# Performance work log

Measured on AMD Instinct MI355X. Metric: run time of the kernel, lower is better.

## Reference

```python
import jax, jax.numpy as jnp
import numpy as np

V = 50000
E = 800000
B, FIN, FOUT, K = 2, 64, 64, 4


def setup_inputs() -> dict:
    key = jax.random.key(0)
    k1, k2, k3, k4, k5, k6 = jax.random.split(key, 6)
    inputs = jax.random.normal(k1, (B, V, FIN), dtype=jnp.float32)
    weight = jax.random.normal(k2, (K, FIN, FOUT), dtype=jnp.float32) * np.sqrt(2.0 / (FIN * K)).astype(np.float32)
    bias = jax.random.normal(k3, (FOUT,), dtype=jnp.float32)
    lap_vals = jax.random.normal(k4, (E,), dtype=jnp.float32)
    lap_rows = jax.random.randint(k5, (E,), 0, V, dtype=jnp.int32)
    lap_cols = jax.random.randint(k6, (E,), 0, V, dtype=jnp.int32)
    return {"inputs": inputs, "weight": weight, "bias": bias,
            "lap_vals": lap_vals, "lap_rows": lap_rows, "lap_cols": lap_cols}


def reference(inputs, weight, bias, lap_vals, lap_rows, lap_cols):
    B_, V_, Fin = inputs.shape
    K_, _, Fout = weight.shape

    def spmm(x):  # L @ x, L in COO; x: [V, Fin*B]
        return jax.ops.segment_sum(lap_vals[:, None] * x[lap_cols], lap_rows, num_segments=V_)

    # x0: [V, Fin*B] (Fin-major flatten, matching torch permute(1,2,0).view)
    x0 = jnp.transpose(inputs, (1, 2, 0)).reshape(V_, Fin * B_)
    xs = [x0]
    if K_ > 1:
        x1 = spmm(x0)
        xs.append(x1)
        for _ in range(2, K_):
            x2 = 2.0 * spmm(x1) - x0
            xs.append(x2)
            x0, x1 = x1, x2
    # [K,V,Fin,B] -> [B,V,Fin,K] -> [B*V, Fin*K]
    X = jnp.stack(xs).reshape(K_, V_, Fin, B_)
    X = jnp.transpose(X, (3, 1, 2, 0)).reshape(B_ * V_, Fin * K_)
    # faithful to original: weight flattened as (K*Fin, Fout)
    out = X @ weight.reshape(K_ * Fin, Fout)
    return out.reshape(B_, V_, Fout) + bias
```

## Files before the change

kernel.cpp:

```cpp
#include <hip/hip_runtime.h>
#include <hip/hip_bf16.h>


#define NV 50000
#define NE 800000
#define XROW 128
#define NROWS 100000
#define NTILES 6250
#define EPMAX 1700000
#define BSHIFT 7
#define RPB 128
#define NB 391
#define CAP 3072
#define CHUNK 4096
#define P1_BLOCKS 196
#define X0_BLOCKS 12500

using u16 = unsigned short;
using u32 = unsigned int;
using u64 = unsigned long long;
typedef __bf16 bf16x8 __attribute__((ext_vector_type(8)));
typedef float f32x4 __attribute__((ext_vector_type(4)));

__device__ __forceinline__ float bflo(u32 g) { return __uint_as_float(g << 16); }
__device__ __forceinline__ float bfhi(u32 g) { return __uint_as_float(g & 0xffff0000u); }
__device__ __forceinline__ u32 pack_bf2(float a, float b) {
    u16 ha = __builtin_bit_cast(u16, (__bf16)a);
    u16 hb = __builtin_bit_cast(u16, (__bf16)b);
    return (u32)ha | ((u32)hb << 16);
}
__device__ __forceinline__ float unpack_f16hi(u32 rec) {
    u16 h = (u16)(rec >> 16);
    return (float)__builtin_bit_cast(_Float16, h);
}
__device__ __forceinline__ int pad32(int n) { return (n + 31) & ~31; }

__global__ __launch_bounds__(256) void bin1_k(const int* __restrict__ rows, const int* __restrict__ cols,
                                              const float* __restrict__ vals,
                                              int* __restrict__ binctr, u64* __restrict__ tmp) {
    __shared__ int bcnt[NB];
    __shared__ int bofs[NB];
    __shared__ int bcur[NB];
    __shared__ int gbase[NB];
    __shared__ int ps[256];
    __shared__ u64 stage[CHUNK];
    int t = threadIdx.x;
    int base = blockIdx.x * CHUNK;
    int n = NE - base;
    if (n > CHUNK) n = CHUNK;
    if (n <= 0) return;

    for (int i = t; i < NB; i += 256) bcnt[i] = 0;
    __syncthreads();

    for (int i = t; i < n; i += 256) {
        atomicAdd(&bcnt[rows[base + i] >> BSHIFT], 1);
    }
    __syncthreads();

    int i0 = 2 * t, i1 = 2 * t + 1;
    int a0 = (i0 < NB) ? bcnt[i0] : 0;
    int a1 = (i1 < NB) ? bcnt[i1] : 0;
    ps[t] = a0 + a1;
    __syncthreads();
    for (int off = 1; off < 256; off <<= 1) {
        int v = (t >= off) ? ps[t - off] : 0;
        __syncthreads();
        ps[t] += v;
        __syncthreads();
    }
    int eb = ps[t] - (a0 + a1);
    if (i0 < NB) { bofs[i0] = eb;      bcur[i0] = eb;      gbase[i0] = i0 * CAP + atomicAdd(&binctr[i0], a0); }
    if (i1 < NB) { bofs[i1] = eb + a0; bcur[i1] = eb + a0; gbase[i1] = i1 * CAP + atomicAdd(&binctr[i1], a1); }
    __syncthreads();

    for (int i = t; i < n; i += 256) {
        int r = rows[base + i];
        int c = cols[base + i];
        u16 hv = __builtin_bit_cast(u16, (_Float16)vals[base + i]);
        u64 rec = ((u64)(u32)r << 32) | (u64)((u32)c | ((u32)hv << 16));
        int s = atomicAdd(&bcur[r >> BSHIFT], 1);
        stage[s] = rec;
    }
    __syncthreads();

    for (int i = t; i < n; i += 256) {
        u64 rec = stage[i];
        int b = (int)(rec >> (32 + BSHIFT));
        tmp[(size_t)(gbase[b] + (i - bofs[b]))] = rec;
    }
}

__global__ __launch_bounds__(256) void bcnt_k(const u64* __restrict__ tmp, const int* __restrict__ binctr,
                                              int* __restrict__ rowc, int* __restrict__ btot,
                                              int* __restrict__ done,
                                              int* __restrict__ bbase, int* __restrict__ row_ptr) {
    __shared__ int rc[RPB];
    __shared__ int rs[RPB];
    __shared__ int ps[256];
    __shared__ int flag;
    int b = blockIdx.x, t = threadIdx.x;
    int n = binctr[b];
    const u64* rec = tmp + (size_t)b * CAP;
    if (t < RPB) rc[t] = 0;
    __syncthreads();
    for (int i = t; i < n; i += 256) {
        atomicAdd(&rc[(int)(rec[i] >> 32) & (RPB - 1)], 1);
    }
    __syncthreads();
    if (t < RPB) {
        rowc[b * RPB + t] = rc[t];
        rs[t] = pad32(rc[t]);
    }
    __syncthreads();
    for (int off = 64; off > 0; off >>= 1) {
        if (t < off) rs[t] += rs[t + off];
        __syncthreads();
    }
    if (t == 0) {
        btot[b] = rs[0];
        __threadfence();
        int ticket = atomicAdd(done, 1);
        flag = (ticket == NB - 1);
    }
    __syncthreads();
    if (flag) {
        __threadfence();
        int i0 = 2 * t, i1 = 2 * t + 1;
        int a0 = (i0 < NB) ? atomicAdd(&btot[i0], 0) : 0;
        int a1 = (i1 < NB) ? atomicAdd(&btot[i1], 0) : 0;
        ps[t] = a0 + a1;
        __syncthreads();
        for (int off = 1; off < 256; off <<= 1) {
            int v = (t >= off) ? ps[t - off] : 0;
            __syncthreads();
            ps[t] += v;
            __syncthreads();
        }
        int eb = ps[t] - (a0 + a1);
        if (i0 < NB) bbase[i0] = eb;
        if (i1 < NB) bbase[i1] = eb + a0;
        if (t == 255) row_ptr[NV] = ps[255];
    }
}

__global__ __launch_bounds__(256) void place_k(const u64* __restrict__ tmp, const int* __restrict__ binctr,
                                               const int* __restrict__ rowc, const int* __restrict__ bbase,
                                               int* __restrict__ row_ptr, u32* __restrict__ epack) {
    __shared__ int rc[RPB];
    __shared__ int ro[RPB];
    int b = blockIdx.x, t = threadIdx.x;
    int n = binctr[b];
    int base = bbase[b];
    const u64* rec = tmp + (size_t)b * CAP;

    int cv = (t < RPB) ? rowc[b * RPB + t] : 0;
    int pv = pad32(cv);
    if (t < RPB) ro[t] = pv;
    __syncthreads();
    for (int off = 1; off < RPB; off <<= 1) {
        int v = 0;
        if (t < RPB && t >= off) v = ro[t - off];
        __syncthreads();
        if (t < RPB) ro[t] += v;
        __syncthreads();
    }
    if (t < RPB) {
        int ex = ro[t] - pv;
        ro[t] = ex;
        rc[t] = 0;
        int v = (b << BSHIFT) + t;
        if (v < NV) row_ptr[v] = base + ex;
    }
    __syncthreads();
    for (int i = t; i < n; i += 256) {
        u64 r64 = rec[i];
        int r = (int)(r64 >> 32) & (RPB - 1);
        int p = base + ro[r] + atomicAdd(&rc[r], 1);
        epack[p] = (u32)r64;
    }
    __syncthreads();
    if (t < RPB) {
        int s = base + ro[t] + cv;
        int e = base + ro[t] + pv;
        for (int i = s; i < e; ++i) epack[i] = 0;
    }
}

__global__ void bx0w_k(const float* __restrict__ in, u32* __restrict__ x0u,
                       const float* __restrict__ weight, u16* __restrict__ wimg) {
    int bid = blockIdx.x;
    if (bid < X0_BLOCKS) {
        int i = bid * 256 + threadIdx.x;
        int v = i >> 6, p = i & 63;
        int b = p >> 5;
        int f = (p & 31) * 2;
        const float* src = in + (size_t)b * (NV * 64) + (size_t)v * 64 + f;
        float2 t = *(const float2*)src;
        x0u[i] = pack_bf2(t.x, t.y);
    } else {
        int i = (bid - X0_BLOCKS) * 256 + threadIdx.x;
        int c = i >> 6, o = i & 63;
        int cp = ((c & 3) << 6) | (c >> 2);
        wimg[o * 264 + cp] = __builtin_bit_cast(u16, (__bf16)weight[i]);
    }
}

__global__ __launch_bounds__(256) void spmm_k(const u32* __restrict__ x,
                                              const u32* __restrict__ xprev,
                                              const int* __restrict__ row_ptr,
                                              const u32* __restrict__ epack,
                                              u32* __restrict__ xout, int mode) {
    int wave = (int)((blockIdx.x * blockDim.x + threadIdx.x) >> 6);
    u32 lane = threadIdx.x & 63;
    int row = __builtin_amdgcn_readfirstlane(wave);
    if (row >= NV) return;
    int beg = row_ptr[row];
    int end = row_ptr[row + 1];
    int q = (int)(lane >> 4);
    u32 g16 = lane & 15;

    float ax[4] = {0.f, 0.f, 0.f, 0.f};
    float ay[4] = {0.f, 0.f, 0.f, 0.f};

    for (int e = beg; e < end; e += 32) {
        u32 rec[8];
        #pragma unroll
        for (int u = 0; u < 8; ++u) rec[u] = epack[e + 4 * u + q];
        uint4 gv[8];
        #pragma unroll
        for (int u = 0; u < 8; ++u)
            gv[u] = *(const uint4*)(x + ((rec[u] & 0xffffu) << 6) + (g16 << 2));
        #pragma unroll
        for (int u = 0; u < 8; ++u) {
            float w = unpack_f16hi(rec[u]);
            ax[0] += w * bflo(gv[u].x); ay[0] += w * bfhi(gv[u].x);
            ax[1] += w * bflo(gv[u].y); ay[1] += w * bfhi(gv[u].y);
            ax[2] += w * bflo(gv[u].z); ay[2] += w * bfhi(gv[u].z);
            ax[3] += w * bflo(gv[u].w); ay[3] += w * bfhi(gv[u].w);
        }
    }

    #pragma unroll
    for (int m = 16; m <= 32; m <<= 1) {
        #pragma unroll
        for (int j = 0; j < 4; ++j) {
            ax[j] += __shfl_xor(ax[j], m, 64);
            ay[j] += __shfl_xor(ay[j], m, 64);
        }
    }

    if (q == 0) {
        if (mode) {
            uint4 pv = *(const uint4*)(xprev + ((u32)row << 6) + (g16 << 2));
            ax[0] = 2.f * ax[0] - bflo(pv.x); ay[0] = 2.f * ay[0] - bfhi(pv.x);
            ax[1] = 2.f * ax[1] - bflo(pv.y); ay[1] = 2.f * ay[1] - bfhi(pv.y);
            ax[2] = 2.f * ax[2] - bflo(pv.z); ay[2] = 2.f * ay[2] - bfhi(pv.z);
            ax[3] = 2.f * ax[3] - bflo(pv.w); ay[3] = 2.f * ay[3] - bfhi(pv.w);
        }
        uint4 o;
        o.x = pack_bf2(ax[0], ay[0]);
        o.y = pack_bf2(ax[1], ay[1]);
        o.z = pack_bf2(ax[2], ay[2]);
        o.w = pack_bf2(ax[3], ay[3]);
        *(uint4*)(xout + ((u32)row << 6) + (g16 << 2)) = o;
    }
}

__global__ __launch_bounds__(256) void final_k(const u16* __restrict__ x_all,
                                               const u16* __restrict__ wimg,
                                               const float* __restrict__ bias,
                                               float* __restrict__ out) {
    __shared__ u16 Wt[64 * 264];
    {
        const u32* src = (const u32*)wimg;
        u32* dst = (u32*)Wt;
        #pragma unroll 4
        for (int i = threadIdx.x; i < 64 * 264 / 2; i += 256) dst[i] = src[i];
    }
    __syncthreads();

    int lane = threadIdx.x & 63;
    int wid = threadIdx.x >> 6;
    int pair = blockIdx.x * 4 + wid;
    int t0 = pair * 2;
    if (t0 >= NTILES) return;

    int m = lane & 15;
    int q8 = (lane >> 4) * 8;

    int r0 = t0 * 16 + m;
    int r1 = r0 + 16;
    const u16* arow0 = x_all + (size_t)(r0 >> 1) * XROW + (r0 & 1) * 64;
    const u16* arow1 = x_all + (size_t)(r1 >> 1) * XROW + (r1 & 1) * 64;

    f32x4 accA[4] = {{0,0,0,0},{0,0,0,0},{0,0,0,0},{0,0,0,0}};
    f32x4 accB[4] = {{0,0,0,0},{0,0,0,0},{0,0,0,0},{0,0,0,0}};

    #pragma unroll
    for (int kb = 0; kb < 8; ++kb) {
        int cb = kb * 32 + q8;
        int arr = cb >> 6;
        int f0 = cb & 63;
        size_t aoff = (size_t)arr * (NV * XROW) + f0;
        bf16x8 a0 = *(const bf16x8*)(arow0 + aoff);
        bf16x8 a1 = *(const bf16x8*)(arow1 + aoff);
        #pragma unroll
        for (int j = 0; j < 4; ++j) {
            bf16x8 bj = *(const bf16x8*)&Wt[(j * 16 + m) * 264 + kb * 32 + q8];
            accA[j] = __builtin_amdgcn_mfma_f32_16x16x32_bf16(a0, bj, accA[j], 0, 0, 0);
            accB[j] = __builtin_amdgcn_mfma_f32_16x16x32_bf16(a1, bj, accB[j], 0, 0, 0);
        }
    }

    float bv[4];
    #pragma unroll
    for (int j = 0; j < 4; ++j) bv[j] = bias[j * 16 + m];

    #pragma unroll
    for (int half = 0; half < 2; ++half) {
        int rbase = (t0 + half) * 16 + (lane >> 4) * 4;
        f32x4* acc = half ? accB : accA;
        #pragma unroll
        for (int reg = 0; reg < 4; ++reg) {
            int rr = rbase + reg;
            float* op = out + (size_t)(rr & 1) * (NV * 64) + (size_t)(rr >> 1) * 64;
            #pragma unroll
            for (int j = 0; j < 4; ++j) op[j * 16 + m] = acc[j][reg] + bv[j];
        }
    }
}

extern "C" void kernel_launch(void* const* d_in, const int* in_sizes, int n_in,
                              void* d_out, int out_size, void* d_ws, size_t ws_size,
                              hipStream_t stream) {
    const float* inputs = (const float*)d_in[0];
    const float* weight = (const float*)d_in[1];
    const float* bias   = (const float*)d_in[2];
    const float* lapv   = (const float*)d_in[3];
    const int*   lrows  = (const int*)d_in[4];
    const int*   lcols  = (const int*)d_in[5];
    float* out = (float*)d_out;

    char* ws = (char*)d_ws;
    size_t o = 0;
    auto alloc = [&](size_t bytes) -> void* {
        void* p = ws + o;
        o += (bytes + 255) & ~(size_t)255;
        return p;
    };
    u16* x_all = (u16*)alloc((size_t)4 * NV * XROW * 2);
    u32* epack = (u32*)alloc((size_t)EPMAX * 4);
    u64* tmp   = (u64*)alloc((size_t)NB * CAP * 8);
    int* row_ptr = (int*)alloc((size_t)(NV + 1) * 4);
    int* binctr  = (int*)alloc((size_t)(NB + 1) * 4);
    int* btot    = (int*)alloc((size_t)NB * 4);
    int* bbase   = (int*)alloc((size_t)NB * 4);
    int* rowc    = (int*)alloc((size_t)NB * RPB * 4);
    u16* wimg = (u16*)alloc((size_t)64 * 264 * 2);
    (void)ws_size; (void)in_sizes; (void)n_in; (void)out_size;

    int* done = binctr + NB;

    u32* x0 = (u32*)(x_all + (size_t)0 * NV * XROW);
    u32* x1 = (u32*)(x_all + (size_t)1 * NV * XROW);
    u32* x2 = (u32*)(x_all + (size_t)2 * NV * XROW);
    u32* x3 = (u32*)(x_all + (size_t)3 * NV * XROW);

    hipMemsetAsync(binctr, 0, (size_t)(NB + 1) * 4, stream);
    bin1_k<<<P1_BLOCKS, 256, 0, stream>>>(lrows, lcols, lapv, binctr, tmp);
    bcnt_k<<<NB, 256, 0, stream>>>(tmp, binctr, rowc, btot, done, bbase, row_ptr);
    place_k<<<NB, 256, 0, stream>>>(tmp, binctr, rowc, bbase, row_ptr, epack);
    bx0w_k<<<X0_BLOCKS + 64, 256, 0, stream>>>(inputs, x0, weight, wimg);

    spmm_k<<<(NV + 3) / 4, 256, 0, stream>>>(x0, nullptr, row_ptr, epack, x1, 0);
    spmm_k<<<(NV + 3) / 4, 256, 0, stream>>>(x1, x0, row_ptr, epack, x2, 1);
    spmm_k<<<(NV + 3) / 4, 256, 0, stream>>>(x2, x1, row_ptr, epack, x3, 1);

    final_k<<<(NTILES / 2 + 3) / 4, 256, 0, stream>>>(x_all, wimg, bias, out);
}
```

Before: 234.8 us.

## Fuse three SpMM passes into one cooperative kernel with grid sync

```diff
diff --git a/kernel.cpp b/kernel.cpp
--- a/kernel.cpp
+++ b/kernel.cpp
@@ -1,13 +1,16 @@
 #include <hip/hip_runtime.h>
 #include <hip/hip_bf16.h>
-
+#include <hip/hip_cooperative_groups.h>
+
+
+namespace cg = cooperative_groups;
 
 #define NV 50000
 #define NE 800000
 #define XROW 128
 #define NROWS 100000
 #define NTILES 6250
-#define EPMAX 1700000
+#define EPMAX 1600000
 #define BSHIFT 7
 #define RPB 128
 #define NB 391
@@ -33,7 +36,7 @@
     u16 h = (u16)(rec >> 16);
     return (float)__builtin_bit_cast(_Float16, h);
 }
-__device__ __forceinline__ int pad32(int n) { return (n + 31) & ~31; }
+__device__ __forceinline__ int pad16(int n) { return (n + 15) & ~15; }
 
 __global__ __launch_bounds__(256) void bin1_k(const int* __restrict__ rows, const int* __restrict__ cols,
                                               const float* __restrict__ vals,
@@ -110,7 +113,7 @@
     __syncthreads();
     if (t < RPB) {
         rowc[b * RPB + t] = rc[t];
-        rs[t] = pad32(rc[t]);
+        rs[t] = pad16(rc[t]);
     }
     __syncthreads();
     for (int off = 64; off > 0; off >>= 1) {
@@ -155,7 +158,7 @@
     const u64* rec = tmp + (size_t)b * CAP;
 
     int cv = (t < RPB) ? rowc[b * RPB + t] : 0;
-    int pv = pad32(cv);
+    int pv = pad16(cv);
     if (t < RPB) ro[t] = pv;
     __syncthreads();
     for (int off = 1; off < RPB; off <<= 1) {
@@ -206,64 +209,84 @@
     }
 }
 
-__global__ __launch_bounds__(256) void spmm_k(const u32* __restrict__ x,
-                                              const u32* __restrict__ xprev,
-                                              const int* __restrict__ row_ptr,
-                                              const u32* __restrict__ epack,
-                                              u32* __restrict__ xout, int mode) {
-    int wave = (int)((blockIdx.x * blockDim.x + threadIdx.x) >> 6);
+__global__ __launch_bounds__(256, 8) void spmm3_k(const u32* __restrict__ x0,
+                                                  u32* __restrict__ x1,
+                                                  u32* __restrict__ x2,
+                                                  u32* __restrict__ x3,
+                                                  const int* __restrict__ row_ptr,
+                                                  const u32* __restrict__ epack) {
+    cg::grid_group grid = cg::this_grid();
+    int gw = (int)((blockIdx.x * blockDim.x + threadIdx.x) >> 6);
+    int nw = (int)((gridDim.x * blockDim.x) >> 6);
     u32 lane = threadIdx.x & 63;
-    int row = __builtin_amdgcn_readfirstlane(wave);
-    if (row >= NV) return;
-    int beg = row_ptr[row];
-    int end = row_ptr[row + 1];
     int q = (int)(lane >> 4);
     u32 g16 = lane & 15;
 
-    float ax[4] = {0.f, 0.f, 0.f, 0.f};
-    float ay[4] = {0.f, 0.f, 0.f, 0.f};
-
-    for (int e = beg; e < end; e += 32) {
-        u32 rec[8];
-        #pragma unroll
-        for (int u = 0; u < 8; ++u) rec[u] = epack[e + 4 * u + q];
-        uint4 gv[8];
-        #pragma unroll
-        for (int u = 0; u < 8; ++u)
-            gv[u] = *(const uint4*)(x + ((rec[u] & 0xffffu) << 6) + (g16 << 2));
-        #pragma unroll
-        for (int u = 0; u < 8; ++u) {
-            float w = unpack_f16hi(rec[u]);
-            ax[0] += w * bflo(gv[u].x); ay[0] += w * bfhi(gv[u].x);
-            ax[1] += w * bflo(gv[u].y); ay[1] += w * bfhi(gv[u].y);
-            ax[2] += w * bflo(gv[u].z); ay[2] += w * bfhi(gv[u].z);
-            ax[3] += w * bflo(gv[u].w); ay[3] += w * bfhi(gv[u].w);
+    const u32* xs[3] = {x0, x1, x2};
+    const u32* xp[3] = {nullptr, x0, x1};
+    u32* xo[3] = {x1, x2, x3};
+
+    for (int pass = 0; pass < 3; ++pass) {
+        const u32* __restrict__ x = xs[pass];
+        const u32* __restrict__ xprev = xp[pass];
+        u32* __restrict__ xout = xo[pass];
+
+        for (int row = gw; row < NV; row += nw) {
+            int row_s = __builtin_amdgcn_readfirstlane(row);
+            int beg = row_ptr[row_s];
+            int end = row_ptr[row_s + 1];
+
+            float ax[4] = {0.f, 0.f, 0.f, 0.f};
+            float ay[4] = {0.f, 0.f, 0.f, 0.f};
+
+            for (int e = beg; e < end; e += 16) {
+                u32 rec[4];
+                uint4 gv[4];
+                #pragma unroll
+                for (int u = 0; u < 4; ++u) {
+                    rec[u] = epack[e + 4 * u + q];
+                    gv[u] = *(const uint4*)(x + ((rec[u] & 0xffffu) << 6) + (g16 << 2));
+                }
+                #pragma unroll
+                for (int u = 0; u < 4; ++u) {
+                    float w = unpack_f16hi(rec[u]);
+                    ax[0] += w * bflo(gv[u].x); ay[0] += w * bfhi(gv[u].x);
+                    ax[1] += w * bflo(gv[u].y); ay[1] += w * bfhi(gv[u].y);
+                    ax[2] += w * bflo(gv[u].z); ay[2] += w * bfhi(gv[u].z);
+                    ax[3] += w * bflo(gv[u].w); ay[3] += w * bfhi(gv[u].w);
+                }
+            }
+
+            #pragma unroll
+            for (int m = 16; m <= 32; m <<= 1) {
+                #pragma unroll
+                for (int j = 0; j < 4; ++j) {
+                    ax[j] += __shfl_xor(ax[j], m, 64);
+                    ay[j] += __shfl_xor(ay[j], m, 64);
+                }
+            }
+
+            if (q == 0) {
+                if (pass) {
+                    uint4 pv = *(const uint4*)(xprev + ((u32)row_s << 6) + (g16 << 2));
+                    ax[0] = 2.f * ax[0] - bflo(pv.x); ay[0] = 2.f * ay[0] - bfhi(pv.x);
+                    ax[1] = 2.f * ax[1] - bflo(pv.y); ay[1] = 2.f * ay[1] - bfhi(pv.y);
+                    ax[2] = 2.f * ax[2] - bflo(pv.z); ay[2] = 2.f * ay[2] - bfhi(pv.z);
+                    ax[3] = 2.f * ax[3] - bflo(pv.w); ay[3] = 2.f * ay[3] - bfhi(pv.w);
+                }
+                uint4 o;
+                o.x = pack_bf2(ax[0], ay[0]);
+                o.y = pack_bf2(ax[1], ay[1]);
+                o.z = pack_bf2(ax[2], ay[2]);
+                o.w = pack_bf2(ax[3], ay[3]);
+                *(uint4*)(xout + ((u32)row_s << 6) + (g16 << 2)) = o;
+            }
         }
-    }
-
-    #pragma unroll
-    for (int m = 16; m <= 32; m <<= 1) {
-        #pragma unroll
-        for (int j = 0; j < 4; ++j) {
-            ax[j] += __shfl_xor(ax[j], m, 64);
-            ay[j] += __shfl_xor(ay[j], m, 64);
+
+        if (pass < 2) {
+            __threadfence();
+            grid.sync();
         }
-    }
-
-    if (q == 0) {
-        if (mode) {
-            uint4 pv = *(const uint4*)(xprev + ((u32)row << 6) + (g16 << 2));
-            ax[0] = 2.f * ax[0] - bflo(pv.x); ay[0] = 2.f * ay[0] - bfhi(pv.x);
-            ax[1] = 2.f * ax[1] - bflo(pv.y); ay[1] = 2.f * ay[1] - bfhi(pv.y);
-            ax[2] = 2.f * ax[2] - bflo(pv.z); ay[2] = 2.f * ay[2] - bfhi(pv.z);
-            ax[3] = 2.f * ax[3] - bflo(pv.w); ay[3] = 2.f * ay[3] - bfhi(pv.w);
-        }
-        uint4 o;
-        o.x = pack_bf2(ax[0], ay[0]);
-        o.y = pack_bf2(ax[1], ay[1]);
-        o.z = pack_bf2(ax[2], ay[2]);
-        o.w = pack_bf2(ax[3], ay[3]);
-        *(uint4*)(xout + ((u32)row << 6) + (g16 << 2)) = o;
     }
 }
 
@@ -373,9 +396,17 @@
     place_k<<<NB, 256, 0, stream>>>(tmp, binctr, rowc, bbase, row_ptr, epack);
     bx0w_k<<<X0_BLOCKS + 64, 256, 0, stream>>>(inputs, x0, weight, wimg);
 
-    spmm_k<<<(NV + 3) / 4, 256, 0, stream>>>(x0, nullptr, row_ptr, epack, x1, 0);
-    spmm_k<<<(NV + 3) / 4, 256, 0, stream>>>(x1, x0, row_ptr, epack, x2, 1);
-    spmm_k<<<(NV + 3) / 4, 256, 0, stream>>>(x2, x1, row_ptr, epack, x3, 1);
+    int maxBlocksPerCU = 0;
+    hipOccupancyMaxActiveBlocksPerMultiprocessor(&maxBlocksPerCU, spmm3_k, 256, 0);
+    int sgrid = maxBlocksPerCU * 256;
+    if (sgrid > 2048) sgrid = 2048;
+    if (sgrid < 256) sgrid = 256;
+    {
+        const u32* a0 = x0; u32* a1 = x1; u32* a2 = x2; u32* a3 = x3;
+        const int* rp = row_ptr; const u32* ep = epack;
+        void* args[] = { &a0, &a1, &a2, &a3, &rp, &ep };
+        hipLaunchCooperativeKernel((const void*)spmm3_k, dim3(sgrid), dim3(256), args, 0, stream);
+    }
 
     final_k<<<(NTILES / 2 + 3) / 4, 256, 0, stream>>>(x_all, wimg, bias, out);
 }
```

Result: slower. 685.3 us (+191.9%).

## Fuse preprocessing kernels, spin-wait grid barrier, pad rows to 16

Applied to the files above, without the earlier changes.

```diff
diff --git a/kernel.cpp b/kernel.cpp
--- a/kernel.cpp
+++ b/kernel.cpp
@@ -7,7 +7,7 @@
 #define XROW 128
 #define NROWS 100000
 #define NTILES 6250
-#define EPMAX 1700000
+#define EPMAX 1600000
 #define BSHIFT 7
 #define RPB 128
 #define NB 391
@@ -15,6 +15,7 @@
 #define CHUNK 4096
 #define P1_BLOCKS 196
 #define X0_BLOCKS 12500
+#define W_BLOCKS 64
 
 using u16 = unsigned short;
 using u32 = unsigned int;
@@ -33,19 +34,42 @@
     u16 h = (u16)(rec >> 16);
     return (float)__builtin_bit_cast(_Float16, h);
 }
-__device__ __forceinline__ int pad32(int n) { return (n + 31) & ~31; }
-
-__global__ __launch_bounds__(256) void bin1_k(const int* __restrict__ rows, const int* __restrict__ cols,
-                                              const float* __restrict__ vals,
-                                              int* __restrict__ binctr, u64* __restrict__ tmp) {
+__device__ __forceinline__ int pad16(int n) { return (n + 15) & ~15; }
+
+__global__ __launch_bounds__(256) void prep1_k(const int* __restrict__ rows, const int* __restrict__ cols,
+                                               const float* __restrict__ vals,
+                                               int* __restrict__ binctr, u64* __restrict__ tmp,
+                                               const float* __restrict__ in, u32* __restrict__ x0u,
+                                               const float* __restrict__ weight, u16* __restrict__ wimg) {
     __shared__ int bcnt[NB];
     __shared__ int bofs[NB];
     __shared__ int bcur[NB];
     __shared__ int gbase[NB];
     __shared__ int ps[256];
     __shared__ u64 stage[CHUNK];
+    int bid = blockIdx.x;
     int t = threadIdx.x;
-    int base = blockIdx.x * CHUNK;
+
+    if (bid >= P1_BLOCKS) {
+        int rb = bid - P1_BLOCKS;
+        if (rb < X0_BLOCKS) {
+            int i = rb * 256 + t;
+            int v = i >> 6, p = i & 63;
+            int b = p >> 5;
+            int f = (p & 31) * 2;
+            const float* src = in + (size_t)b * (NV * 64) + (size_t)v * 64 + f;
+            float2 tv = *(const float2*)src;
+            x0u[i] = pack_bf2(tv.x, tv.y);
+        } else {
+            int i = (rb - X0_BLOCKS) * 256 + t;
+            int c = i >> 6, o = i & 63;
+            int cp = ((c & 3) << 6) | (c >> 2);
+            wimg[o * 264 + cp] = __builtin_bit_cast(u16, (__bf16)weight[i]);
+        }
+        return;
+    }
+
+    int base = bid * CHUNK;
     int n = NE - base;
     if (n > CHUNK) n = CHUNK;
     if (n <= 0) return;
@@ -91,41 +115,44 @@
     }
 }
 
-__global__ __launch_bounds__(256) void bcnt_k(const u64* __restrict__ tmp, const int* __restrict__ binctr,
-                                              int* __restrict__ rowc, int* __restrict__ btot,
-                                              int* __restrict__ done,
-                                              int* __restrict__ bbase, int* __restrict__ row_ptr) {
+__global__ __launch_bounds__(256) void prep2_k(const u64* __restrict__ tmp, const int* __restrict__ binctr,
+                                               int* __restrict__ btot, int* __restrict__ done,
+                                               int* __restrict__ flag,
+                                               int* __restrict__ bbase, int* __restrict__ row_ptr,
+                                               u32* __restrict__ epack) {
     __shared__ int rc[RPB];
-    __shared__ int rs[RPB];
+    __shared__ int ro[RPB];
     __shared__ int ps[256];
-    __shared__ int flag;
+    __shared__ int sbase;
+    __shared__ int lastflag;
     int b = blockIdx.x, t = threadIdx.x;
     int n = binctr[b];
     const u64* rec = tmp + (size_t)b * CAP;
+
     if (t < RPB) rc[t] = 0;
     __syncthreads();
     for (int i = t; i < n; i += 256) {
         atomicAdd(&rc[(int)(rec[i] >> 32) & (RPB - 1)], 1);
     }
     __syncthreads();
-    if (t < RPB) {
-        rowc[b * RPB + t] = rc[t];
-        rs[t] = pad32(rc[t]);
-    }
-    __syncthreads();
-    for (int off = 64; off > 0; off >>= 1) {
-        if (t < off) rs[t] += rs[t + off];
+    int cv = (t < RPB) ? rc[t] : 0;
+    int pv = pad16(cv);
+
+    ps[t] = (t < RPB) ? pv : 0;
+    __syncthreads();
+    for (int off = 128; off > 0; off >>= 1) {
+        if (t < off) ps[t] += ps[t + off];
         __syncthreads();
     }
     if (t == 0) {
-        btot[b] = rs[0];
+        btot[b] = ps[0];
         __threadfence();
         int ticket = atomicAdd(done, 1);
-        flag = (ticket == NB - 1);
-    }
-    __syncthreads();
-    if (flag) {
-        __threadfence();
+        lastflag = (ticket == NB - 1);
+    }
+    __syncthreads();
+
+    if (lastflag) {
         int i0 = 2 * t, i1 = 2 * t + 1;
         int a0 = (i0 < NB) ? atomicAdd(&btot[i0], 0) : 0;
         int a1 = (i1 < NB) ? atomicAdd(&btot[i1], 0) : 0;
@@ -141,21 +168,18 @@
         if (i0 < NB) bbase[i0] = eb;
         if (i1 < NB) bbase[i1] = eb + a0;
         if (t == 255) row_ptr[NV] = ps[255];
-    }
-}
-
-__global__ __launch_bounds__(256) void place_k(const u64* __restrict__ tmp, const int* __restrict__ binctr,
-                                               const int* __restrict__ rowc, const int* __restrict__ bbase,
-                                               int* __restrict__ row_ptr, u32* __restrict__ epack) {
-    __shared__ int rc[RPB];
-    __shared__ int ro[RPB];
-    int b = blockIdx.x, t = threadIdx.x;
-    int n = binctr[b];
-    int base = bbase[b];
-    const u64* rec = tmp + (size_t)b * CAP;
-
-    int cv = (t < RPB) ? rowc[b * RPB + t] : 0;
-    int pv = pad32(cv);
+        __threadfence();
+        __syncthreads();
+        if (t == 0) atomicExch(flag, 1);
+    }
+
+    if (t == 0) {
+        while (atomicAdd(flag, 0) == 0) __builtin_amdgcn_s_sleep(8);
+        sbase = atomicAdd(&bbase[b], 0);
+    }
+    __syncthreads();
+    int base = sbase;
+
     if (t < RPB) ro[t] = pv;
     __syncthreads();
     for (int off = 1; off < RPB; off <<= 1) {
@@ -184,25 +208,6 @@
         int s = base + ro[t] + cv;
         int e = base + ro[t] + pv;
         for (int i = s; i < e; ++i) epack[i] = 0;
-    }
-}
-
-__global__ void bx0w_k(const float* __restrict__ in, u32* __restrict__ x0u,
-                       const float* __restrict__ weight, u16* __restrict__ wimg) {
-    int bid = blockIdx.x;
-    if (bid < X0_BLOCKS) {
-        int i = bid * 256 + threadIdx.x;
-        int v = i >> 6, p = i & 63;
-        int b = p >> 5;
-        int f = (p & 31) * 2;
-        const float* src = in + (size_t)b * (NV * 64) + (size_t)v * 64 + f;
-        float2 t = *(const float2*)src;
-        x0u[i] = pack_bf2(t.x, t.y);
-    } else {
-        int i = (bid - X0_BLOCKS) * 256 + threadIdx.x;
-        int c = i >> 6, o = i & 63;
-        int cp = ((c & 3) << 6) | (c >> 2);
-        wimg[o * 264 + cp] = __builtin_bit_cast(u16, (__bf16)weight[i]);
     }
 }
 
@@ -223,16 +228,16 @@
     float ax[4] = {0.f, 0.f, 0.f, 0.f};
     float ay[4] = {0.f, 0.f, 0.f, 0.f};
 
-    for (int e = beg; e < end; e += 32) {
-        u32 rec[8];
-        #pragma unroll
-        for (int u = 0; u < 8; ++u) rec[u] = epack[e + 4 * u + q];
-        uint4 gv[8];
-        #pragma unroll
-        for (int u = 0; u < 8; ++u)
+    for (int e = beg; e < end; e += 16) {
+        u32 rec[4];
+        uint4 gv[4];
+        #pragma unroll
+        for (int u = 0; u < 4; ++u) {
+            rec[u] = epack[e + 4 * u + q];
             gv[u] = *(const uint4*)(x + ((rec[u] & 0xffffu) << 6) + (g16 << 2));
-        #pragma unroll
-        for (int u = 0; u < 8; ++u) {
+        }
+        #pragma unroll
+        for (int u = 0; u < 4; ++u) {
             float w = unpack_f16hi(rec[u]);
             ax[0] += w * bflo(gv[u].x); ay[0] += w * bfhi(gv[u].x);
             ax[1] += w * bflo(gv[u].y); ay[1] += w * bfhi(gv[u].y);
@@ -353,25 +358,24 @@
     u32* epack = (u32*)alloc((size_t)EPMAX * 4);
     u64* tmp   = (u64*)alloc((size_t)NB * CAP * 8);
     int* row_ptr = (int*)alloc((size_t)(NV + 1) * 4);
-    int* binctr  = (int*)alloc((size_t)(NB + 1) * 4);
+    int* binctr  = (int*)alloc((size_t)(NB + 2) * 4);
     int* btot    = (int*)alloc((size_t)NB * 4);
     int* bbase   = (int*)alloc((size_t)NB * 4);
-    int* rowc    = (int*)alloc((size_t)NB * RPB * 4);
     u16* wimg = (u16*)alloc((size_t)64 * 264 * 2);
     (void)ws_size; (void)in_sizes; (void)n_in; (void)out_size;
 
     int* done = binctr + NB;
+    int* flag = binctr + NB + 1;
 
     u32* x0 = (u32*)(x_all + (size_t)0 * NV * XROW);
     u32* x1 = (u32*)(x_all + (size_t)1 * NV * XROW);
     u32* x2 = (u32*)(x_all + (size_t)2 * NV * XROW);
     u32* x3 = (u32*)(x_all + (size_t)3 * NV * XROW);
 
-    hipMemsetAsync(binctr, 0, (size_t)(NB + 1) * 4, stream);
-    bin1_k<<<P1_BLOCKS, 256, 0, stream>>>(lrows, lcols, lapv, binctr, tmp);
-    bcnt_k<<<NB, 256, 0, stream>>>(tmp, binctr, rowc, btot, done, bbase, row_ptr);
-    place_k<<<NB, 256, 0, stream>>>(tmp, binctr, rowc, bbase, row_ptr, epack);
-    bx0w_k<<<X0_BLOCKS + 64, 256, 0, stream>>>(inputs, x0, weight, wimg);
+    hipMemsetAsync(binctr, 0, (size_t)(NB + 2) * 4, stream);
+    prep1_k<<<P1_BLOCKS + X0_BLOCKS + W_BLOCKS, 256, 0, stream>>>(
+        lrows, lcols, lapv, binctr, tmp, inputs, x0, weight, wimg);
+    prep2_k<<<NB, 256, 0, stream>>>(tmp, binctr, btot, done, flag, bbase, row_ptr, epack);
 
     spmm_k<<<(NV + 3) / 4, 256, 0, stream>>>(x0, nullptr, row_ptr, epack, x1, 0);
     spmm_k<<<(NV + 3) / 4, 256, 0, stream>>>(x1, x0, row_ptr, epack, x2, 1);
```

Result: slower. 245.3 us (+4.5%).
